# Kernel optimization log

Hardware: AMD Instinct MI355X
Metric: run time of the kernel (lower is better)

Reference implementation:

```python
import jax, jax.numpy as jnp
import numpy as np

TEMPERATURE = 0.1  # init kwarg
EPS = 1e-8        # torch cosine_similarity eps


def setup_inputs() -> dict:
    key = jax.random.key(0)
    k1, k2, k3 = jax.random.split(key, 3)
    B, D, C = 4096, 1024, 32
    representations = jax.random.normal(k1, (B, D), dtype=jnp.float32)
    soft_labels = jax.random.uniform(k2, (B, C), dtype=jnp.float32)
    labels = jax.random.randint(k3, (B,), 0, 32, dtype=jnp.int64)
    return {
        "representations": representations,
        "soft_labels": soft_labels,
        "labels": labels,
        "pseudo_weight": 10,
    }


def reference(representations, soft_labels, labels, pseudo_weight):
    B = representations.shape[0]
    # row-normalize (cosine similarity)
    norms = jnp.maximum(jnp.linalg.norm(representations, axis=1, keepdims=True), EPS)
    rn = representations / norms
    Z = (rn @ rn.T) / TEMPERATURE                      # [B, B] scaled cosine sims
    E = jnp.exp(Z)
    off_diag = 1.0 - jnp.eye(B, dtype=Z.dtype)         # exclude j == i
    denom = jnp.sum(E * off_diag, axis=1, keepdims=True)   # [B, 1]
    loss_arr = -(Z - jnp.log(denom))                   # -log(exp(Z_ij)/denom_i)
    # positive-pair weights: same label, j != i (detached in original)
    pos = (labels[:, None] == labels[None, :]).astype(Z.dtype) * off_diag
    soft_sim = jax.lax.stop_gradient(soft_labels @ soft_labels.T)  # torch.inner, detached
    w = pos + pseudo_weight * soft_sim
    return jnp.sum(loss_arr * w) / B
```

## Files before the change

kernel.cpp:

```cpp
#include <hip/hip_runtime.h>
#include <hip/hip_bf16.h>
#include <stdint.h>


typedef float f32x4 __attribute__((ext_vector_type(4)));
typedef float f32x2 __attribute__((ext_vector_type(2)));
typedef long i64;

#define INV_T 10.0f
#define Z_SCALE (INV_T / 256.0f)

#define GLD16(gp, lp)                                                          \
    __builtin_amdgcn_global_load_lds(                                          \
        (const __attribute__((address_space(1))) uint32_t*)(gp),               \
        (__attribute__((address_space(3))) uint32_t*)(lp), 16, 0, 0)

#define OFF_RNF8  0
#define OFF_DENOM 4194304
#define OFF_POSS  (OFF_DENOM + 16384)
#define OFF_G     (OFF_POSS + 16384)
#define OFF_OACC  (OFF_G + 131072)
#define OFF_DONE  (OFF_OACC + 16)
#define ZERO_SPAN 167936
#define OFF_CSP   (OFF_DENOM + ZERO_SPAN)
#define OFF_CCP   (OFF_CSP + 4096)
#define OFF_W     (OFF_CCP + 4096)

__global__ __launch_bounds__(256) void scl_stage1(const float* __restrict__ rep,
                                                  const float* __restrict__ sl,
                                                  const int* __restrict__ labels,
                                                  uint32_t* __restrict__ rnf8,
                                                  float* __restrict__ cs_part,
                                                  int* __restrict__ cc_part,
                                                  char* __restrict__ zbase) {
    int b = blockIdx.x;
    int t = threadIdx.x;
    if (b < 4096) {
        int row = b;
        const float4* src = reinterpret_cast<const float4*>(rep + (size_t)row * 1024);
        float4 v = src[t];
        float s = v.x * v.x + v.y * v.y + v.z * v.z + v.w * v.w;
#pragma unroll
        for (int m = 1; m < 64; m <<= 1) s += __shfl_xor(s, m, 64);
        __shared__ float red[4];
        if ((t & 63) == 0) red[t >> 6] = s;
        __syncthreads();
        s = red[0] + red[1] + red[2] + red[3];
        float nf = 16.0f / fmaxf(sqrtf(s), 1e-8f);
        int p = 0;
        p = __builtin_amdgcn_cvt_pk_fp8_f32(v.x * nf, v.y * nf, p, false);
        p = __builtin_amdgcn_cvt_pk_fp8_f32(v.z * nf, v.w * nf, p, true);
        rnf8[row * 256 + t] = (uint32_t)p;
    } else if (b < 4128) {
        __shared__ float part[8][32];
        __shared__ int bins[32];
        int bb = b - 4096;
        if (t < 32) bins[t] = 0;
        __syncthreads();
        if (t < 128) atomicAdd(&bins[labels[bb * 128 + t]], 1);
        int c = t & 31, rg = t >> 5;
        float s = 0.f;
#pragma unroll 4
        for (int k = 0; k < 16; ++k) {
            int i = bb * 128 + rg * 16 + k;
            s += sl[i * 32 + c];
        }
        part[rg][c] = s;
        __syncthreads();
        if (t < 32) {
            float tot = 0.f;
#pragma unroll
            for (int g = 0; g < 8; ++g) tot += part[g][t];
            cs_part[bb * 32 + t] = tot;
            cc_part[bb * 32 + t] = bins[t];
        }
    } else {
        int zb = b - 4128;
        *(uint4*)(zbase + (size_t)zb * 4096 + t * 16) = (uint4){0, 0, 0, 0};
    }
}

__global__ __launch_bounds__(256) void scl_main(const uint8_t* __restrict__ rnf8,
                                                const float* __restrict__ sl,
                                                const int* __restrict__ labels,
                                                const float* __restrict__ cs_part,
                                                const int* __restrict__ cc_part,
                                                const int* __restrict__ pwp,
                                                float* __restrict__ denom,
                                                float* __restrict__ posS,
                                                float* __restrict__ G,
                                                float* __restrict__ W) {
    int tid = threadIdx.x;

    if (blockIdx.x >= 528) {
        if (blockIdx.x < 1040) {
            int idx = blockIdx.x - 528;
            int dblk = idx & 15, ks = idx >> 4;
            int dq = tid >> 5, c = tid & 31;
            int d0 = dblk * 64 + dq * 8;
            f32x2 acc2[4];
#pragma unroll
            for (int j = 0; j < 4; ++j) acc2[j] = (f32x2){0.f, 0.f};
            int i0 = ks * 128;
#pragma unroll 4
            for (int k = 0; k < 128; ++k) {
                int i = i0 + k;
                uint2 rv = *(const uint2*)&rnf8[(size_t)i * 1024 + d0];
                float sv = sl[i * 32 + c];
                f32x2 sv2 = {sv, sv};
                acc2[0] += __builtin_amdgcn_cvt_pk_f32_fp8((int)rv.x, false) * sv2;
                acc2[1] += __builtin_amdgcn_cvt_pk_f32_fp8((int)rv.x, true) * sv2;
                acc2[2] += __builtin_amdgcn_cvt_pk_f32_fp8((int)rv.y, false) * sv2;
                acc2[3] += __builtin_amdgcn_cvt_pk_f32_fp8((int)rv.y, true) * sv2;
            }
#pragma unroll
            for (int j = 0; j < 4; ++j) {
                atomicAdd(&G[(d0 + 2 * j) * 32 + c], acc2[j][0] * 0.0625f);
                atomicAdd(&G[(d0 + 2 * j + 1) * 32 + c], acc2[j][1] * 0.0625f);
            }
        } else {
            __shared__ __align__(16) float css[32];
            __shared__ int ccs[32];
            if (tid < 32) {
                float s = 0.f; int n = 0;
#pragma unroll
                for (int b = 0; b < 32; ++b) { s += cs_part[b * 32 + tid]; n += cc_part[b * 32 + tid]; }
                css[tid] = s; ccs[tid] = n;
            }
            __syncthreads();
            int bits = *pwp;
            float pw = (bits >= -(1 << 22) && bits <= (1 << 22)) ? (float)bits
                                                                 : __int_as_float(bits);
            int i = (blockIdx.x - 1040) * 256 + tid;
            const f32x4* sl4 = (const f32x4*)sl;
            const f32x4* cs4 = (const f32x4*)css;
            float dW = 0.f;
#pragma unroll
            for (int q = 0; q < 8; ++q) {
                f32x4 s = sl4[i * 8 + q];
                f32x4 c = cs4[q];
                dW += s[0] * c[0] + s[1] * c[1] + s[2] * c[2] + s[3] * c[3];
            }
            W[i] = (float)(ccs[labels[i]] - 1) + pw * dW;
        }
        return;
    }

    __shared__ __align__(16) uint8_t As[2 * 128 * 64];
    __shared__ __align__(16) uint8_t Bs[2 * 128 * 64];
    __shared__ int lblA[128], lblB[128];

    int L = blockIdx.x;
    int bi = 0, rem = L;
    while (rem >= 32 - bi) { rem -= 32 - bi; ++bi; }
    int bj = bi + rem;
    int rowA0 = bi * 128, colB0 = bj * 128;

    if (tid < 128) {
        lblA[tid] = labels[rowA0 + tid];
        lblB[tid] = labels[colB0 + tid];
    }

    int lane = tid & 63, warp = tid >> 6;
    int wr = warp >> 1, wc = warp & 1;
    int m_ = lane & 15, g = lane >> 4;

    int r4 = lane >> 2;
    int csw = (lane & 3) ^ ((lane >> 3) & 3);
    const uint8_t* gA0 = rnf8 + (size_t)(rowA0 + warp * 32 + r4) * 1024 + csw * 16;
    const uint8_t* gB0 = rnf8 + (size_t)(colB0 + warp * 32 + r4) * 1024 + csw * 16;

    f32x4 acc[4][4];
#pragma unroll
    for (int a = 0; a < 4; ++a)
#pragma unroll
        for (int b = 0; b < 4; ++b) acc[a][b] = (f32x4){0.f, 0.f, 0.f, 0.f};

    int fsw = (g ^ ((m_ >> 1) & 3)) * 16;

    GLD16(gA0,         &As[(warp * 32) * 64]);
    GLD16(gA0 + 16384, &As[(warp * 32 + 16) * 64]);
    GLD16(gB0,         &Bs[(warp * 32) * 64]);
    GLD16(gB0 + 16384, &Bs[(warp * 32 + 16) * 64]);

    for (int kt = 0; kt < 16; ++kt) {
        __syncthreads();
        int cb = (kt & 1) * 8192, nb = 8192 - cb;
        if (kt < 15) {
            GLD16(gA0 + (kt + 1) * 64,         &As[nb + (warp * 32) * 64]);
            GLD16(gA0 + (kt + 1) * 64 + 16384, &As[nb + (warp * 32 + 16) * 64]);
            GLD16(gB0 + (kt + 1) * 64,         &Bs[nb + (warp * 32) * 64]);
            GLD16(gB0 + (kt + 1) * 64 + 16384, &Bs[nb + (warp * 32 + 16) * 64]);
        }
        f32x4 aq[4], bq[4];
#pragma unroll
        for (int ti = 0; ti < 4; ++ti) {
            int rowLoc = wr * 64 + ti * 16 + m_;
            aq[ti] = *(const f32x4*)&As[cb + rowLoc * 64 + fsw];
        }
#pragma unroll
        for (int tj = 0; tj < 4; ++tj) {
            int colLoc = wc * 64 + tj * 16 + m_;
            bq[tj] = *(const f32x4*)&Bs[cb + colLoc * 64 + fsw];
        }
#pragma unroll
        for (int s = 0; s < 2; ++s)
#pragma unroll
            for (int ti = 0; ti < 4; ++ti)
#pragma unroll
                for (int tj = 0; tj < 4; ++tj) {
                    i64 a = ((const i64*)&aq[ti])[s];
                    i64 b = ((const i64*)&bq[tj])[s];
                    acc[ti][tj] = __builtin_amdgcn_mfma_f32_16x16x32_fp8_fp8(
                        a, b, acc[ti][tj], 0, 0, 0);
                }
    }

    bool isDiag = (bi == bj);
    int cl = m_;
    float colE[4] = {0.f, 0.f, 0.f, 0.f}, colP[4] = {0.f, 0.f, 0.f, 0.f};
#pragma unroll
    for (int ti = 0; ti < 4; ++ti) {
        int rowLoc = wr * 64 + ti * 16 + g * 4;
        float rE[4] = {0.f, 0.f, 0.f, 0.f}, rP[4] = {0.f, 0.f, 0.f, 0.f};
        int lr[4];
#pragma unroll
        for (int r = 0; r < 4; ++r) lr[r] = lblA[rowLoc + r];
#pragma unroll
        for (int tj = 0; tj < 4; ++tj) {
            int colLoc = wc * 64 + tj * 16 + cl;
            int gCol = colB0 + colLoc;
            int lc = lblB[colLoc];
            f32x4 a = acc[ti][tj];
#pragma unroll
            for (int r = 0; r < 4; ++r) {
                int gRow = rowA0 + rowLoc + r;
                float z = Z_SCALE * a[r];
                float e = __expf(z);
                bool offd = (gRow != gCol);
                if (!offd) e = 0.f;
                rE[r] += e;
                colE[tj] += e;
                if (offd && (lr[r] == lc)) { rP[r] += z; colP[tj] += z; }
            }
        }
#pragma unroll
        for (int r = 0; r < 4; ++r) {
            float v = rE[r], p = rP[r];
#pragma unroll
            for (int msk = 1; msk < 16; msk <<= 1) {
                v += __shfl_xor(v, msk, 64);
                p += __shfl_xor(p, msk, 64);
            }
            if (cl == 0) {
                int gRow = rowA0 + rowLoc + r;
                atomicAdd(&denom[gRow], v);
                atomicAdd(&posS[gRow], p);
            }
        }
    }
    if (!isDiag) {
#pragma unroll
        for (int tj = 0; tj < 4; ++tj) {
            float v = colE[tj], p = colP[tj];
            v += __shfl_xor(v, 16, 64); p += __shfl_xor(p, 16, 64);
            v += __shfl_xor(v, 32, 64); p += __shfl_xor(p, 32, 64);
            if (g == 0) {
                int gCol = colB0 + wc * 64 + tj * 16 + cl;
                atomicAdd(&denom[gCol], v);
                atomicAdd(&posS[gCol], p);
            }
        }
    }
}

__global__ __launch_bounds__(256) void scl_finalize(const float* __restrict__ denom,
                                                    const float* __restrict__ posS,
                                                    const float* __restrict__ W,
                                                    const float* __restrict__ G,
                                                    const int* __restrict__ pwp,
                                                    double* __restrict__ oacc,
                                                    int* __restrict__ done,
                                                    float* __restrict__ out) {
    int t = threadIdx.x;
    __shared__ double wsum[4];
    double contrib = 0.0;

    if (blockIdx.x < 8) {
        int i0 = blockIdx.x * 512 + t;
        float t0 = __logf(denom[i0]) * W[i0] - posS[i0];
        float t1 = __logf(denom[i0 + 256]) * W[i0 + 256] - posS[i0 + 256];
        double td = (double)t0 + (double)t1;
#pragma unroll
        for (int m = 1; m < 64; m <<= 1) td += __shfl_xor(td, m, 64);
        if ((t & 63) == 0) wsum[t >> 6] = td;
        __syncthreads();
        contrib = wsum[0] + wsum[1] + wsum[2] + wsum[3];
    } else {
        int bits = *pwp;
        float pw = (bits >= -(1 << 22) && bits <= (1 << 22)) ? (float)bits
                                                             : __int_as_float(bits);
        const f32x4* G4 = (const f32x4*)G;
        float gs = 0.f;
#pragma unroll
        for (int q = 0; q < 32; ++q) {
            f32x4 v = G4[q * 256 + t];
            gs += v[0] * v[0] + v[1] * v[1] + v[2] * v[2] + v[3] * v[3];
        }
        double gd = (double)gs;
#pragma unroll
        for (int m = 1; m < 64; m <<= 1) gd += __shfl_xor(gd, m, 64);
        if ((t & 63) == 0) wsum[t >> 6] = gd;
        __syncthreads();
        contrib = -(double)(pw * INV_T) * (wsum[0] + wsum[1] + wsum[2] + wsum[3]);
    }

    if (t == 0) {
        atomicAdd(oacc, contrib);
        __threadfence();
        int old = atomicAdd(done, 1);
        if (old == 8) {
            double tot = atomicAdd(oacc, 0.0);
            out[0] = (float)(tot * (1.0 / 4096.0));
        }
    }
}

extern "C" void kernel_launch(void* const* d_in, const int* in_sizes, int n_in,
                              void* d_out, int out_size, void* d_ws, size_t ws_size,
                              hipStream_t stream) {
    const float* rep = (const float*)d_in[0];
    const float* sl = (const float*)d_in[1];
    const int* labels = (const int*)d_in[2];
    const int* pwp = (const int*)d_in[3];

    char* ws = (char*)d_ws;
    uint8_t* rnf8 = (uint8_t*)(ws + OFF_RNF8);
    float* denom = (float*)(ws + OFF_DENOM);
    float* posS = (float*)(ws + OFF_POSS);
    float* G = (float*)(ws + OFF_G);
    double* oacc = (double*)(ws + OFF_OACC);
    int* done = (int*)(ws + OFF_DONE);
    float* cs_part = (float*)(ws + OFF_CSP);
    int* cc_part = (int*)(ws + OFF_CCP);
    float* W = (float*)(ws + OFF_W);

    scl_stage1<<<4169, 256, 0, stream>>>(rep, sl, labels, (uint32_t*)rnf8,
                                         cs_part, cc_part, ws + OFF_DENOM);
    scl_main<<<1056, 256, 0, stream>>>(rnf8, sl, labels, cs_part, cc_part, pwp,
                                       denom, posS, G, W);
    scl_finalize<<<9, 256, 0, stream>>>(denom, posS, W, G, pwp, oacc, done,
                                        (float*)d_out);
}
```

Measured before the change: 118.3 us.

## Shrink Gram tiles to single-wave 64x64 blocks and move W into finalize

The main FP8 MFMA Gram kernel now runs one 64-thread wave per 64x64 upper-triangular tile instead of four waves per 128x128 tile. It replaces __syncthreads with explicit vmcnt waits on a double-buffered LDS pipeline and reads labels straight from global memory. The G side-branch uses 16-byte loads with 64-thread blocks, and the per-row weight W is now computed inside finalize rather than in extra blocks of the main kernel. The aim is to remove block-level barriers, raise occupancy and wave count, and drop the W round trip. The cost is roughly twice the global and LDS operand traffic per output, since reuse per tile is halved.

```diff
diff --git a/kernel.cpp b/kernel.cpp
--- a/kernel.cpp
+++ b/kernel.cpp
@@ -24,7 +24,6 @@
 #define ZERO_SPAN 167936
 #define OFF_CSP   (OFF_DENOM + ZERO_SPAN)
 #define OFF_CCP   (OFF_CSP + 4096)
-#define OFF_W     (OFF_CCP + 4096)
 
 __global__ __launch_bounds__(256) void scl_stage1(const float* __restrict__ rep,
                                                   const float* __restrict__ sl,
@@ -80,95 +79,75 @@
     }
 }
 
-__global__ __launch_bounds__(256) void scl_main(const uint8_t* __restrict__ rnf8,
-                                                const float* __restrict__ sl,
-                                                const int* __restrict__ labels,
-                                                const float* __restrict__ cs_part,
-                                                const int* __restrict__ cc_part,
-                                                const int* __restrict__ pwp,
-                                                float* __restrict__ denom,
-                                                float* __restrict__ posS,
-                                                float* __restrict__ G,
-                                                float* __restrict__ W) {
-    int tid = threadIdx.x;
-
-    if (blockIdx.x >= 528) {
-        if (blockIdx.x < 1040) {
-            int idx = blockIdx.x - 528;
-            int dblk = idx & 15, ks = idx >> 4;
-            int dq = tid >> 5, c = tid & 31;
-            int d0 = dblk * 64 + dq * 8;
-            f32x2 acc2[4];
-#pragma unroll
-            for (int j = 0; j < 4; ++j) acc2[j] = (f32x2){0.f, 0.f};
-            int i0 = ks * 128;
-#pragma unroll 4
-            for (int k = 0; k < 128; ++k) {
-                int i = i0 + k;
-                uint2 rv = *(const uint2*)&rnf8[(size_t)i * 1024 + d0];
-                float sv = sl[i * 32 + c];
-                f32x2 sv2 = {sv, sv};
-                acc2[0] += __builtin_amdgcn_cvt_pk_f32_fp8((int)rv.x, false) * sv2;
-                acc2[1] += __builtin_amdgcn_cvt_pk_f32_fp8((int)rv.x, true) * sv2;
-                acc2[2] += __builtin_amdgcn_cvt_pk_f32_fp8((int)rv.y, false) * sv2;
-                acc2[3] += __builtin_amdgcn_cvt_pk_f32_fp8((int)rv.y, true) * sv2;
-            }
-#pragma unroll
-            for (int j = 0; j < 4; ++j) {
-                atomicAdd(&G[(d0 + 2 * j) * 32 + c], acc2[j][0] * 0.0625f);
-                atomicAdd(&G[(d0 + 2 * j + 1) * 32 + c], acc2[j][1] * 0.0625f);
-            }
-        } else {
-            __shared__ __align__(16) float css[32];
-            __shared__ int ccs[32];
-            if (tid < 32) {
-                float s = 0.f; int n = 0;
-#pragma unroll
-                for (int b = 0; b < 32; ++b) { s += cs_part[b * 32 + tid]; n += cc_part[b * 32 + tid]; }
-                css[tid] = s; ccs[tid] = n;
-            }
-            __syncthreads();
-            int bits = *pwp;
-            float pw = (bits >= -(1 << 22) && bits <= (1 << 22)) ? (float)bits
-                                                                 : __int_as_float(bits);
-            int i = (blockIdx.x - 1040) * 256 + tid;
-            const f32x4* sl4 = (const f32x4*)sl;
-            const f32x4* cs4 = (const f32x4*)css;
-            float dW = 0.f;
-#pragma unroll
-            for (int q = 0; q < 8; ++q) {
-                f32x4 s = sl4[i * 8 + q];
-                f32x4 c = cs4[q];
-                dW += s[0] * c[0] + s[1] * c[1] + s[2] * c[2] + s[3] * c[3];
-            }
-            W[i] = (float)(ccs[labels[i]] - 1) + pw * dW;
+__global__ __launch_bounds__(64) void scl_main(const uint8_t* __restrict__ rnf8,
+                                               const float* __restrict__ sl,
+                                               const int* __restrict__ labels,
+                                               float* __restrict__ denom,
+                                               float* __restrict__ posS,
+                                               float* __restrict__ G) {
+    int lane = threadIdx.x;
+
+    if (blockIdx.x >= 2080) {
+        int u = blockIdx.x - 2080;
+        int dblk = u & 31, ks = u >> 5;
+        int c = lane & 31, dq = lane >> 5;
+        int d0 = dblk * 32 + dq * 16;
+        f32x2 acc2[8];
+#pragma unroll
+        for (int j = 0; j < 8; ++j) acc2[j] = (f32x2){0.f, 0.f};
+        int i0 = ks * 128;
+#pragma unroll 2
+        for (int k = 0; k < 128; ++k) {
+            int i = i0 + k;
+            uint4 rv = *(const uint4*)&rnf8[(size_t)i * 1024 + d0];
+            float sv = sl[i * 32 + c];
+            f32x2 sv2 = {sv, sv};
+            acc2[0] += __builtin_amdgcn_cvt_pk_f32_fp8((int)rv.x, false) * sv2;
+            acc2[1] += __builtin_amdgcn_cvt_pk_f32_fp8((int)rv.x, true) * sv2;
+            acc2[2] += __builtin_amdgcn_cvt_pk_f32_fp8((int)rv.y, false) * sv2;
+            acc2[3] += __builtin_amdgcn_cvt_pk_f32_fp8((int)rv.y, true) * sv2;
+            acc2[4] += __builtin_amdgcn_cvt_pk_f32_fp8((int)rv.z, false) * sv2;
+            acc2[5] += __builtin_amdgcn_cvt_pk_f32_fp8((int)rv.z, true) * sv2;
+            acc2[6] += __builtin_amdgcn_cvt_pk_f32_fp8((int)rv.w, false) * sv2;
+            acc2[7] += __builtin_amdgcn_cvt_pk_f32_fp8((int)rv.w, true) * sv2;
+        }
+#pragma unroll
+        for (int j = 0; j < 8; ++j) {
+            atomicAdd(&G[(d0 + 2 * j) * 32 + c], acc2[j][0] * 0.0625f);
+            atomicAdd(&G[(d0 + 2 * j + 1) * 32 + c], acc2[j][1] * 0.0625f);
         }
         return;
     }
 
-    __shared__ __align__(16) uint8_t As[2 * 128 * 64];
-    __shared__ __align__(16) uint8_t Bs[2 * 128 * 64];
-    __shared__ int lblA[128], lblB[128];
+    __shared__ __align__(16) uint8_t Ls[16384];
 
     int L = blockIdx.x;
     int bi = 0, rem = L;
-    while (rem >= 32 - bi) { rem -= 32 - bi; ++bi; }
+    while (rem >= 64 - bi) { rem -= 64 - bi; ++bi; }
     int bj = bi + rem;
-    int rowA0 = bi * 128, colB0 = bj * 128;
-
-    if (tid < 128) {
-        lblA[tid] = labels[rowA0 + tid];
-        lblB[tid] = labels[colB0 + tid];
-    }
-
-    int lane = tid & 63, warp = tid >> 6;
-    int wr = warp >> 1, wc = warp & 1;
+    int rowA0 = bi * 64, colB0 = bj * 64;
+
     int m_ = lane & 15, g = lane >> 4;
-
     int r4 = lane >> 2;
     int csw = (lane & 3) ^ ((lane >> 3) & 3);
-    const uint8_t* gA0 = rnf8 + (size_t)(rowA0 + warp * 32 + r4) * 1024 + csw * 16;
-    const uint8_t* gB0 = rnf8 + (size_t)(colB0 + warp * 32 + r4) * 1024 + csw * 16;
+    const uint8_t* gA = rnf8 + (size_t)(rowA0 + r4) * 1024 + csw * 16;
+    const uint8_t* gB = rnf8 + (size_t)(colB0 + r4) * 1024 + csw * 16;
+    uint8_t* As = Ls;
+    uint8_t* Bs = Ls + 4096;
+
+#define ISSUE8(KT, NB)                                                         \
+    {                                                                          \
+        const uint8_t* pa = gA + (KT) * 64;                                    \
+        const uint8_t* pb = gB + (KT) * 64;                                    \
+        GLD16(pa,          As + (NB));                                         \
+        GLD16(pa + 16384,  As + (NB) + 1024);                                  \
+        GLD16(pa + 32768,  As + (NB) + 2048);                                  \
+        GLD16(pa + 49152,  As + (NB) + 3072);                                  \
+        GLD16(pb,          Bs + (NB));                                         \
+        GLD16(pb + 16384,  Bs + (NB) + 1024);                                  \
+        GLD16(pb + 32768,  Bs + (NB) + 2048);                                  \
+        GLD16(pb + 49152,  Bs + (NB) + 3072);                                  \
+    }
 
     f32x4 acc[4][4];
 #pragma unroll
@@ -178,31 +157,23 @@
 
     int fsw = (g ^ ((m_ >> 1) & 3)) * 16;
 
-    GLD16(gA0,         &As[(warp * 32) * 64]);
-    GLD16(gA0 + 16384, &As[(warp * 32 + 16) * 64]);
-    GLD16(gB0,         &Bs[(warp * 32) * 64]);
-    GLD16(gB0 + 16384, &Bs[(warp * 32 + 16) * 64]);
-
+    ISSUE8(0, 0);
+#pragma unroll
     for (int kt = 0; kt < 16; ++kt) {
-        __syncthreads();
-        int cb = (kt & 1) * 8192, nb = 8192 - cb;
+        int cb = (kt & 1) * 8192;
         if (kt < 15) {
-            GLD16(gA0 + (kt + 1) * 64,         &As[nb + (warp * 32) * 64]);
-            GLD16(gA0 + (kt + 1) * 64 + 16384, &As[nb + (warp * 32 + 16) * 64]);
-            GLD16(gB0 + (kt + 1) * 64,         &Bs[nb + (warp * 32) * 64]);
-            GLD16(gB0 + (kt + 1) * 64 + 16384, &Bs[nb + (warp * 32 + 16) * 64]);
+            ISSUE8(kt + 1, 8192 - cb);
+            asm volatile("s_waitcnt vmcnt(8)" ::: "memory");
+        } else {
+            asm volatile("s_waitcnt vmcnt(0)" ::: "memory");
         }
         f32x4 aq[4], bq[4];
 #pragma unroll
-        for (int ti = 0; ti < 4; ++ti) {
-            int rowLoc = wr * 64 + ti * 16 + m_;
-            aq[ti] = *(const f32x4*)&As[cb + rowLoc * 64 + fsw];
-        }
-#pragma unroll
-        for (int tj = 0; tj < 4; ++tj) {
-            int colLoc = wc * 64 + tj * 16 + m_;
-            bq[tj] = *(const f32x4*)&Bs[cb + colLoc * 64 + fsw];
-        }
+        for (int ti = 0; ti < 4; ++ti)
+            aq[ti] = *(const f32x4*)&As[cb + (ti * 16 + m_) * 64 + fsw];
+#pragma unroll
+        for (int tj = 0; tj < 4; ++tj)
+            bq[tj] = *(const f32x4*)&Bs[cb + (tj * 16 + m_) * 64 + fsw];
 #pragma unroll
         for (int s = 0; s < 2; ++s)
 #pragma unroll
@@ -215,22 +186,25 @@
                         a, b, acc[ti][tj], 0, 0, 0);
                 }
     }
+#undef ISSUE8
 
     bool isDiag = (bi == bj);
     int cl = m_;
     float colE[4] = {0.f, 0.f, 0.f, 0.f}, colP[4] = {0.f, 0.f, 0.f, 0.f};
+    int lcj[4];
+#pragma unroll
+    for (int tj = 0; tj < 4; ++tj) lcj[tj] = labels[colB0 + tj * 16 + cl];
 #pragma unroll
     for (int ti = 0; ti < 4; ++ti) {
-        int rowLoc = wr * 64 + ti * 16 + g * 4;
+        int rowLoc = ti * 16 + g * 4;
         float rE[4] = {0.f, 0.f, 0.f, 0.f}, rP[4] = {0.f, 0.f, 0.f, 0.f};
         int lr[4];
 #pragma unroll
-        for (int r = 0; r < 4; ++r) lr[r] = lblA[rowLoc + r];
+        for (int r = 0; r < 4; ++r) lr[r] = labels[rowA0 + rowLoc + r];
 #pragma unroll
         for (int tj = 0; tj < 4; ++tj) {
-            int colLoc = wc * 64 + tj * 16 + cl;
-            int gCol = colB0 + colLoc;
-            int lc = lblB[colLoc];
+            int gCol = colB0 + tj * 16 + cl;
+            int lc = lcj[tj];
             f32x4 a = acc[ti][tj];
 #pragma unroll
             for (int r = 0; r < 4; ++r) {
@@ -266,7 +240,7 @@
             v += __shfl_xor(v, 16, 64); p += __shfl_xor(p, 16, 64);
             v += __shfl_xor(v, 32, 64); p += __shfl_xor(p, 32, 64);
             if (g == 0) {
-                int gCol = colB0 + wc * 64 + tj * 16 + cl;
+                int gCol = colB0 + tj * 16 + cl;
                 atomicAdd(&denom[gCol], v);
                 atomicAdd(&posS[gCol], p);
             }
@@ -276,30 +250,57 @@
 
 __global__ __launch_bounds__(256) void scl_finalize(const float* __restrict__ denom,
                                                     const float* __restrict__ posS,
-                                                    const float* __restrict__ W,
+                                                    const float* __restrict__ sl,
+                                                    const int* __restrict__ labels,
+                                                    const float* __restrict__ cs_part,
+                                                    const int* __restrict__ cc_part,
                                                     const float* __restrict__ G,
                                                     const int* __restrict__ pwp,
                                                     double* __restrict__ oacc,
                                                     int* __restrict__ done,
                                                     float* __restrict__ out) {
     int t = threadIdx.x;
+    int bits = *pwp;
+    float pw = (bits >= -(1 << 22) && bits <= (1 << 22)) ? (float)bits
+                                                         : __int_as_float(bits);
     __shared__ double wsum[4];
     double contrib = 0.0;
 
     if (blockIdx.x < 8) {
-        int i0 = blockIdx.x * 512 + t;
-        float t0 = __logf(denom[i0]) * W[i0] - posS[i0];
-        float t1 = __logf(denom[i0 + 256]) * W[i0 + 256] - posS[i0 + 256];
-        double td = (double)t0 + (double)t1;
+        __shared__ __align__(16) float css[32];
+        __shared__ int ccs[32];
+        if (t < 32) {
+            float s = 0.f; int n = 0;
+#pragma unroll
+            for (int b = 0; b < 32; ++b) {
+                s += cs_part[b * 32 + t];
+                n += cc_part[b * 32 + t];
+            }
+            css[t] = s; ccs[t] = n;
+        }
+        __syncthreads();
+        const f32x4* sl4 = (const f32x4*)sl;
+        const f32x4* cs4 = (const f32x4*)css;
+        double td = 0.0;
+#pragma unroll
+        for (int h = 0; h < 2; ++h) {
+            int i = blockIdx.x * 512 + h * 256 + t;
+            float dW = 0.f;
+#pragma unroll
+            for (int q = 0; q < 8; ++q) {
+                f32x4 s = sl4[i * 8 + q];
+                f32x4 c = cs4[q];
+                dW += s[0] * c[0] + s[1] * c[1] + s[2] * c[2] + s[3] * c[3];
+            }
+            float Wv = (float)(ccs[labels[i]] - 1) + pw * dW;
+            td += (double)(__logf(denom[i]) * Wv - posS[i]);
+        }
 #pragma unroll
         for (int m = 1; m < 64; m <<= 1) td += __shfl_xor(td, m, 64);
         if ((t & 63) == 0) wsum[t >> 6] = td;
         __syncthreads();
         contrib = wsum[0] + wsum[1] + wsum[2] + wsum[3];
     } else {
-        int bits = *pwp;
-        float pw = (bits >= -(1 << 22) && bits <= (1 << 22)) ? (float)bits
-                                                             : __int_as_float(bits);
         const f32x4* G4 = (const f32x4*)G;
         float gs = 0.f;
 #pragma unroll
@@ -343,12 +344,10 @@
     int* done = (int*)(ws + OFF_DONE);
     float* cs_part = (float*)(ws + OFF_CSP);
     int* cc_part = (int*)(ws + OFF_CCP);
-    float* W = (float*)(ws + OFF_W);
 
     scl_stage1<<<4169, 256, 0, stream>>>(rep, sl, labels, (uint32_t*)rnf8,
                                          cs_part, cc_part, ws + OFF_DENOM);
-    scl_main<<<1056, 256, 0, stream>>>(rnf8, sl, labels, cs_part, cc_part, pwp,
-                                       denom, posS, G, W);
-    scl_finalize<<<9, 256, 0, stream>>>(denom, posS, W, G, pwp, oacc, done,
-                                        (float*)d_out);
+    scl_main<<<3104, 64, 0, stream>>>(rnf8, sl, labels, denom, posS, G);
+    scl_finalize<<<9, 256, 0, stream>>>(denom, posS, sl, labels, cs_part, cc_part,
+                                        G, pwp, oacc, done, (float*)d_out);
 }
```

Measured after the change: 125.3 us. 1.06x slower.
